# Kernel tuning notes

Measured on AMD Instinct MI355X. Metric: run time of the kernel, lower is better.

Reference implementation:

```python
import jax, jax.numpy as jnp
import numpy as np

B, S, E, H = 4, 2048, 1024, 16
D = E // H  # head dim


def setup_inputs() -> dict:
    key = jax.random.key(0)
    ks = jax.random.split(key, 6)
    sc = 1.0 / np.sqrt(E)
    return {
        "x":  jax.random.normal(ks[0], (B, S, E), dtype=jnp.float32),
        "Wk": jax.random.normal(ks[1], (E, E), dtype=jnp.float32) * sc,
        "Wq": jax.random.normal(ks[2], (E, E), dtype=jnp.float32) * sc,
        "Wv": jax.random.normal(ks[3], (E, E), dtype=jnp.float32) * sc,
        "Wo": jax.random.normal(ks[4], (E, E), dtype=jnp.float32) * sc,
        "bo": jax.random.normal(ks[5], (E,), dtype=jnp.float32) * sc,
    }


def reference(x, Wk, Wq, Wv, Wo, bo):
    b, s, e = x.shape
    # torch Linear: y = x @ W.T (weights are [out, in])
    K = x @ Wk.T
    Q = x @ Wq.T
    _V_unused = x @ Wv.T  # computed in source but discarded (V = Q.view bug)
    # split heads: [b, s, H, D] -> [b, H, s, D]
    Kh = K.reshape(b, s, H, D).transpose(0, 2, 1, 3)
    Qh = Q.reshape(b, s, H, D).transpose(0, 2, 1, 3)
    Vh = Qh  # faithful to source: V = Q.view(...)
    # scaled dot product, scaled by sqrt(embedding_size) as in source
    scores = jnp.einsum('bhqd,bhkd->bhqk', Qh, Kh) / jnp.sqrt(jnp.float32(e))
    causal = jnp.tril(jnp.ones((s, s), dtype=bool))
    scores = jnp.where(causal, scores, -jnp.inf)
    probs = jax.nn.softmax(scores, axis=-1)
    attn = jnp.einsum('bhqk,bhkd->bhqd', probs, Vh)
    attn = attn.transpose(0, 2, 1, 3).reshape(b, s, e)
    return attn @ Wo.T + bo
```

## Files before the change

kernel.cpp:

```cpp
#include <hip/hip_runtime.h>
#include <hip/hip_bf16.h>

#define PB 4
#define PS 2048
#define PE 1024
#define PH 16
#define PD 64

typedef __attribute__((ext_vector_type(8))) short bf16x8;
typedef __attribute__((ext_vector_type(4))) float f32x4;
typedef const __attribute__((address_space(1))) unsigned int* gas_t;
typedef __attribute__((address_space(3))) unsigned int* las_t;

__device__ __forceinline__ unsigned short f2bf(float f) {
  union { float f; unsigned int u; } v;
  v.f = f;
  unsigned int u = v.u;
  u += 0x7fffu + ((u >> 16) & 1u);
  return (unsigned short)(u >> 16);
}

__device__ __forceinline__ f32x4 mfma16(bf16x8 a, bf16x8 b, f32x4 c) {
  return __builtin_amdgcn_mfma_f32_16x16x32_bf16(a, b, c, 0, 0, 0);
}

#define CVT_GROUPS ((PB * PS * PE + 3 * PE * PE) / 4)
#define CVT_BLOCKS (CVT_GROUPS / 256)
__global__ __launch_bounds__(256) void cvt_kernel(
    const float* __restrict__ x, const float* __restrict__ wk,
    const float* __restrict__ wq, const float* __restrict__ wo,
    unsigned short* __restrict__ xb, unsigned short* __restrict__ wkb,
    unsigned short* __restrict__ wqb, unsigned short* __restrict__ wob) {
  const long long NX = (long long)PB * PS * PE;
  const long long NW = (long long)PE * PE;
  long long i = ((long long)blockIdx.x * 256 + threadIdx.x) * 4;
  const float* src;
  unsigned short* dst;
  long long off;
  if (i < NX)               { src = x;  dst = xb;  off = i; }
  else if (i < NX + NW)     { src = wk; dst = wkb; off = i - NX; }
  else if (i < NX + 2 * NW) { src = wq; dst = wqb; off = i - NX - NW; }
  else                      { src = wo; dst = wob; off = i - NX - 2 * NW; }
  float4 v = *(const float4*)(src + off);
  ushort4 o;
  o.x = f2bf(v.x); o.y = f2bf(v.y); o.z = f2bf(v.z); o.w = f2bf(v.w);
  *(ushort4*)(dst + off) = o;
}

__global__ __launch_bounds__(256) void gemm_qk(
    const unsigned short* __restrict__ A, const unsigned short* __restrict__ Bq,
    const unsigned short* __restrict__ Bk,
    unsigned short* __restrict__ QT, unsigned short* __restrict__ Kb) {
  const int K = PE, N = PE;
  __shared__ __attribute__((aligned(16))) unsigned short As[128 * 64];
  __shared__ __attribute__((aligned(16))) unsigned short Bqs[128 * 64];
  __shared__ __attribute__((aligned(16))) unsigned short Bks[128 * 64];
  const int tid = threadIdx.x;
  const int wave = tid >> 6, lane = tid & 63;
  const int quad = lane >> 4, ln = lane & 15;
  const int m0 = blockIdx.y * 128, n0 = blockIdx.x * 128;
  const int wm = (wave >> 1) * 64, wn = (wave & 1) * 64;

  f32x4 aq[4][4], ak[4][4];
#pragma unroll
  for (int i = 0; i < 4; ++i)
#pragma unroll
    for (int j = 0; j < 4; ++j)
#pragma unroll
      for (int r = 0; r < 4; ++r) { aq[i][j][r] = 0.f; ak[i][j][r] = 0.f; }

  for (int k0 = 0; k0 < K; k0 += 64) {
#pragma unroll
    for (int it = 0; it < 4; ++it) {
      const int idx = it * 256 + tid;
      const int row = idx >> 3, ch = idx & 7;
      const int gch = ch ^ (row & 7);
      __builtin_amdgcn_global_load_lds(
          (gas_t)(const void*)(A + (size_t)(m0 + row) * K + k0 + gch * 8),
          (las_t)(void*)((char*)As + idx * 16), 16, 0, 0);
      __builtin_amdgcn_global_load_lds(
          (gas_t)(const void*)(Bq + (size_t)(n0 + row) * K + k0 + gch * 8),
          (las_t)(void*)((char*)Bqs + idx * 16), 16, 0, 0);
      __builtin_amdgcn_global_load_lds(
          (gas_t)(const void*)(Bk + (size_t)(n0 + row) * K + k0 + gch * 8),
          (las_t)(void*)((char*)Bks + idx * 16), 16, 0, 0);
    }
    __syncthreads();
#pragma unroll
    for (int kc = 0; kc < 2; ++kc) {
      bf16x8 af[4], bqf[4], bkf[4];
#pragma unroll
      for (int t = 0; t < 4; ++t) {
        const int ra = wm + t * 16 + ln;
        const int rb = wn + t * 16 + ln;
        af[t]  = *(const bf16x8*)(As  + ra * 64 + ((kc * 4 + quad) ^ (ra & 7)) * 8);
        bqf[t] = *(const bf16x8*)(Bqs + rb * 64 + ((kc * 4 + quad) ^ (rb & 7)) * 8);
        bkf[t] = *(const bf16x8*)(Bks + rb * 64 + ((kc * 4 + quad) ^ (rb & 7)) * 8);
      }
#pragma unroll
      for (int mt = 0; mt < 4; ++mt)
#pragma unroll
        for (int nt = 0; nt < 4; ++nt) {
          aq[mt][nt] = mfma16(af[mt], bqf[nt], aq[mt][nt]);
          ak[mt][nt] = mfma16(af[mt], bkf[nt], ak[mt][nt]);
        }
    }
    __syncthreads();
  }

#pragma unroll
  for (int mt = 0; mt < 4; ++mt) {
#pragma unroll
    for (int nt = 0; nt < 4; ++nt) {
      const int row = m0 + wm + mt * 16 + quad * 4;
      const int col = n0 + wn + nt * 16 + ln;
      const int b = row >> 11, s = row & 2047;
      const int h = col >> 6, d = col & 63;
      ushort4 ov;
      ov.x = f2bf(aq[mt][nt][0]); ov.y = f2bf(aq[mt][nt][1]);
      ov.z = f2bf(aq[mt][nt][2]); ov.w = f2bf(aq[mt][nt][3]);
      *(ushort4*)(QT + (((size_t)(b * PH + h) * PD + d) * PS + s)) = ov;
#pragma unroll
      for (int r = 0; r < 4; ++r)
        Kb[(size_t)(row + r) * N + col] = f2bf(ak[mt][nt][r]);
    }
  }
}

__global__ __launch_bounds__(256) void gemm_out(
    const unsigned short* __restrict__ A, const unsigned short* __restrict__ Bm,
    const float* __restrict__ bias, float* __restrict__ Cf) {
  const int K = PE, N = PE;
  __shared__ __attribute__((aligned(16))) unsigned short As[128 * 64];
  __shared__ __attribute__((aligned(16))) unsigned short Bs[128 * 64];
  const int tid = threadIdx.x;
  const int wave = tid >> 6, lane = tid & 63;
  const int quad = lane >> 4, ln = lane & 15;
  const int m0 = blockIdx.y * 128, n0 = blockIdx.x * 128;
  const int wm = (wave >> 1) * 64, wn = (wave & 1) * 64;

  f32x4 acc[4][4];
#pragma unroll
  for (int i = 0; i < 4; ++i)
#pragma unroll
    for (int j = 0; j < 4; ++j)
#pragma unroll
      for (int r = 0; r < 4; ++r) acc[i][j][r] = 0.f;

  for (int k0 = 0; k0 < K; k0 += 64) {
#pragma unroll
    for (int it = 0; it < 4; ++it) {
      const int idx = it * 256 + tid;
      const int row = idx >> 3, ch = idx & 7;
      const int gch = ch ^ (row & 7);
      __builtin_amdgcn_global_load_lds(
          (gas_t)(const void*)(A + (size_t)(m0 + row) * K + k0 + gch * 8),
          (las_t)(void*)((char*)As + idx * 16), 16, 0, 0);
      __builtin_amdgcn_global_load_lds(
          (gas_t)(const void*)(Bm + (size_t)(n0 + row) * K + k0 + gch * 8),
          (las_t)(void*)((char*)Bs + idx * 16), 16, 0, 0);
    }
    __syncthreads();
#pragma unroll
    for (int kc = 0; kc < 2; ++kc) {
      bf16x8 af[4], bfr[4];
#pragma unroll
      for (int t = 0; t < 4; ++t) {
        const int ra = wm + t * 16 + ln;
        const int rb = wn + t * 16 + ln;
        af[t]  = *(const bf16x8*)(As + ra * 64 + ((kc * 4 + quad) ^ (ra & 7)) * 8);
        bfr[t] = *(const bf16x8*)(Bs + rb * 64 + ((kc * 4 + quad) ^ (rb & 7)) * 8);
      }
#pragma unroll
      for (int mt = 0; mt < 4; ++mt)
#pragma unroll
        for (int nt = 0; nt < 4; ++nt)
          acc[mt][nt] = mfma16(af[mt], bfr[nt], acc[mt][nt]);
    }
    __syncthreads();
  }

#pragma unroll
  for (int mt = 0; mt < 4; ++mt) {
#pragma unroll
    for (int nt = 0; nt < 4; ++nt) {
      const int row = m0 + wm + mt * 16 + quad * 4;
      const int col = n0 + wn + nt * 16 + ln;
      const float bv = bias[col];
#pragma unroll
      for (int r = 0; r < 4; ++r)
        Cf[(size_t)(row + r) * N + col] = acc[mt][nt][r] + bv;
    }
  }
}

__global__ __launch_bounds__(256) void attn_kernel(
    const unsigned short* __restrict__ QT,
    const unsigned short* __restrict__ Kb,
    unsigned short* __restrict__ Ab) {
  __shared__ __attribute__((aligned(16))) unsigned short Ks[64 * 64];
  __shared__ __attribute__((aligned(16))) unsigned short Vs[64 * 64];
  __shared__ __attribute__((aligned(16))) unsigned short Ps[4][32 * 72];

  const int tid = threadIdx.x;
  const int wave = tid >> 6, lane = tid & 63;
  const int quad = lane >> 4, ln = lane & 15;
  const int h = blockIdx.y, b = blockIdx.z;
  const size_t hoff  = ((size_t)b * PS) * PE + (size_t)h * PD;
  const size_t hofft = ((size_t)(b * PH + h) * PD) * PS;
  const float CEXP = 0.045084220f;
  const int srow = tid >> 3, sch = tid & 7;

  for (int pass = 0; pass < 2; ++pass) {
    const int qt = pass ? (int)blockIdx.x : 15 - (int)blockIdx.x;
    const int qw0 = qt * 128 + wave * 32;

    bf16x8 qfr[2][2];
#pragma unroll
    for (int nq = 0; nq < 2; ++nq)
#pragma unroll
      for (int c = 0; c < 2; ++c) {
        union { unsigned short u[8]; bf16x8 v; } tmp;
#pragma unroll
        for (int j = 0; j < 8; ++j)
          tmp.u[j] = QT[hofft + (size_t)(c * 32 + quad * 8 + j) * PS +
                        qw0 + nq * 16 + ln];
        qfr[nq][c] = tmp.v;
      }

    f32x4 o[2][4];
    float psum[2];
#pragma unroll
    for (int mq = 0; mq < 2; ++mq)
#pragma unroll
      for (int td = 0; td < 4; ++td)
#pragma unroll
        for (int r = 0; r < 4; ++r) o[mq][td][r] = 0.f;
    psum[0] = psum[1] = 0.f;

    const int ktend = 2 * qt + 2;
    for (int kt = 0; kt < ktend; ++kt) {
      const int k0 = kt * 64;

#pragma unroll
      for (int r = 0; r < 2; ++r) {
        const int row = r * 32 + srow;
        const int gch = sch ^ (row & 7);
        __builtin_amdgcn_global_load_lds(
            (gas_t)(const void*)(Kb + hoff + (size_t)(k0 + row) * PE + gch * 8),
            (las_t)(void*)((char*)Ks + (r * 256 + tid) * 16), 16, 0, 0);
        __builtin_amdgcn_global_load_lds(
            (gas_t)(const void*)(QT + hofft + (size_t)row * PS + k0 + gch * 8),
            (las_t)(void*)((char*)Vs + (r * 256 + tid) * 16), 16, 0, 0);
      }
      __syncthreads();

      f32x4 sacc[4][2];
#pragma unroll
      for (int mk = 0; mk < 4; ++mk)
#pragma unroll
        for (int nq = 0; nq < 2; ++nq)
#pragma unroll
          for (int r = 0; r < 4; ++r) sacc[mk][nq][r] = 0.f;
#pragma unroll
      for (int c = 0; c < 2; ++c) {
        const int ch = ((c * 4 + quad) ^ (ln & 7)) * 8;
        bf16x8 kf[4];
#pragma unroll
        for (int mk = 0; mk < 4; ++mk)
          kf[mk] = *(const bf16x8*)(Ks + (mk * 16 + ln) * 64 + ch);
#pragma unroll
        for (int mk = 0; mk < 4; ++mk)
#pragma unroll
          for (int nq = 0; nq < 2; ++nq)
            sacc[mk][nq] = mfma16(kf[mk], qfr[nq][c], sacc[mk][nq]);
      }

      const bool edge = (k0 + 63) > qw0;
#pragma unroll
      for (int mk = 0; mk < 4; ++mk)
#pragma unroll
        for (int nq = 0; nq < 2; ++nq) {
          float p[4];
#pragma unroll
          for (int r = 0; r < 4; ++r)
            p[r] = __builtin_amdgcn_exp2f(sacc[mk][nq][r] * CEXP);
          if (edge) {
            const int qg = qw0 + nq * 16 + ln;
#pragma unroll
            for (int r = 0; r < 4; ++r) {
              const int kg = k0 + mk * 16 + quad * 4 + r;
              p[r] = (kg <= qg) ? p[r] : 0.f;
            }
          }
          psum[nq] += (p[0] + p[1]) + (p[2] + p[3]);
          union { __hip_bfloat162 h2; unsigned int u; } u01, u23;
          u01.h2 = __float22bfloat162_rn(float2{p[0], p[1]});
          u23.h2 = __float22bfloat162_rn(float2{p[2], p[3]});
          *(uint2*)(&Ps[wave][(nq * 16 + ln) * 72 + mk * 16 + quad * 4]) =
              uint2{u01.u, u23.u};
        }

#pragma unroll
      for (int c = 0; c < 2; ++c) {
        const int ch = ((c * 4 + quad) ^ (ln & 7)) * 8;
        bf16x8 pf0 = *(const bf16x8*)(&Ps[wave][ln * 72 + c * 32 + quad * 8]);
        bf16x8 pf1 = *(const bf16x8*)(&Ps[wave][(16 + ln) * 72 + c * 32 + quad * 8]);
#pragma unroll
        for (int td = 0; td < 4; ++td) {
          bf16x8 vfd = *(const bf16x8*)(Vs + (td * 16 + ln) * 64 + ch);
          o[0][td] = mfma16(pf0, vfd, o[0][td]);
          o[1][td] = mfma16(pf1, vfd, o[1][td]);
        }
      }
      __syncthreads();
    }

#pragma unroll
    for (int nq = 0; nq < 2; ++nq) {
      psum[nq] += __shfl_xor(psum[nq], 16, 64);
      psum[nq] += __shfl_xor(psum[nq], 32, 64);
    }
    float invq[2][4];
#pragma unroll
    for (int mq = 0; mq < 2; ++mq)
#pragma unroll
      for (int r = 0; r < 4; ++r)
        invq[mq][r] = 1.f / __shfl(psum[mq], quad * 4 + r, 64);

#pragma unroll
    for (int mq = 0; mq < 2; ++mq)
#pragma unroll
      for (int r = 0; r < 4; ++r) {
        const int qg = qw0 + mq * 16 + quad * 4 + r;
#pragma unroll
        for (int td = 0; td < 4; ++td)
          Ab[hoff + (size_t)qg * PE + td * 16 + ln] =
              f2bf(o[mq][td][r] * invq[mq][r]);
      }
  }
}

extern "C" void kernel_launch(void* const* d_in, const int* in_sizes, int n_in,
                              void* d_out, int out_size, void* d_ws, size_t ws_size,
                              hipStream_t stream) {
  (void)in_sizes; (void)n_in; (void)out_size; (void)ws_size;
  const float* x  = (const float*)d_in[0];
  const float* Wk = (const float*)d_in[1];
  const float* Wq = (const float*)d_in[2];
  const float* Wo = (const float*)d_in[4];
  const float* bo = (const float*)d_in[5];
  float* out = (float*)d_out;

  char* ws = (char*)d_ws;
  unsigned short* xb  = (unsigned short*)(ws);
  unsigned short* wkb = (unsigned short*)(ws + (16u << 20));
  unsigned short* wqb = (unsigned short*)(ws + (18u << 20));
  unsigned short* wob = (unsigned short*)(ws + (20u << 20));
  unsigned short* QT  = (unsigned short*)(ws + (22u << 20));
  unsigned short* Kb  = (unsigned short*)(ws + (38u << 20));
  unsigned short* Ab  = xb;

  const int M = PB * PS;

  cvt_kernel<<<dim3(CVT_BLOCKS), dim3(256), 0, stream>>>(
      x, Wk, Wq, Wo, xb, wkb, wqb, wob);

  gemm_qk<<<dim3(PE / 128, M / 128), dim3(256), 0, stream>>>(
      xb, wqb, wkb, QT, Kb);

  attn_kernel<<<dim3(8, PH, PB), dim3(256), 0, stream>>>(QT, Kb, Ab);

  gemm_out<<<dim3(PE / 128, M / 128), dim3(256), 0, stream>>>(
      Ab, wob, bo, out);
}
```

Baseline: 262.0 us.

## Double-buffer LDS tiles in GEMM and attention kernels to overlap loads

Adds ping-pong shared-memory buffers to the QK projection GEMM, the output GEMM, and the attention loop, so the next tile's global-to-LDS load is issued before the current tile is computed. One barrier per iteration replaces the two it had before. The GEMMs halve their K-step to 32 with a new 4-chunk swizzle, which keeps LDS size the same but doubles the iteration count. Attention LDS grows, which may reduce occupancy.

```diff
diff --git a/kernel.cpp b/kernel.cpp
--- a/kernel.cpp
+++ b/kernel.cpp
@@ -52,9 +52,9 @@
     const unsigned short* __restrict__ Bk,
     unsigned short* __restrict__ QT, unsigned short* __restrict__ Kb) {
   const int K = PE, N = PE;
-  __shared__ __attribute__((aligned(16))) unsigned short As[128 * 64];
-  __shared__ __attribute__((aligned(16))) unsigned short Bqs[128 * 64];
-  __shared__ __attribute__((aligned(16))) unsigned short Bks[128 * 64];
+  __shared__ __attribute__((aligned(16))) unsigned short As[2][128 * 32];
+  __shared__ __attribute__((aligned(16))) unsigned short Bqs[2][128 * 32];
+  __shared__ __attribute__((aligned(16))) unsigned short Bks[2][128 * 32];
   const int tid = threadIdx.x;
   const int wave = tid >> 6, lane = tid & 63;
   const int quad = lane >> 4, ln = lane & 15;
@@ -69,43 +69,49 @@
 #pragma unroll
       for (int r = 0; r < 4; ++r) { aq[i][j][r] = 0.f; ak[i][j][r] = 0.f; }
 
-  for (int k0 = 0; k0 < K; k0 += 64) {
-#pragma unroll
-    for (int it = 0; it < 4; ++it) {
+  auto stage = [&](int k0, int bufi) {
+#pragma unroll
+    for (int it = 0; it < 2; ++it) {
       const int idx = it * 256 + tid;
-      const int row = idx >> 3, ch = idx & 7;
-      const int gch = ch ^ (row & 7);
+      const int row = it * 64 + (tid >> 2), ch = tid & 3;
+      const int gch = ch ^ ((row >> 1) & 3);
       __builtin_amdgcn_global_load_lds(
           (gas_t)(const void*)(A + (size_t)(m0 + row) * K + k0 + gch * 8),
-          (las_t)(void*)((char*)As + idx * 16), 16, 0, 0);
+          (las_t)(void*)((char*)As[bufi] + idx * 16), 16, 0, 0);
       __builtin_amdgcn_global_load_lds(
           (gas_t)(const void*)(Bq + (size_t)(n0 + row) * K + k0 + gch * 8),
-          (las_t)(void*)((char*)Bqs + idx * 16), 16, 0, 0);
+          (las_t)(void*)((char*)Bqs[bufi] + idx * 16), 16, 0, 0);
       __builtin_amdgcn_global_load_lds(
           (gas_t)(const void*)(Bk + (size_t)(n0 + row) * K + k0 + gch * 8),
-          (las_t)(void*)((char*)Bks + idx * 16), 16, 0, 0);
-    }
+          (las_t)(void*)((char*)Bks[bufi] + idx * 16), 16, 0, 0);
+    }
+  };
+
+  stage(0, 0);
+  for (int k0 = 0, kit = 0; k0 < K; k0 += 32, ++kit) {
     __syncthreads();
-#pragma unroll
-    for (int kc = 0; kc < 2; ++kc) {
-      bf16x8 af[4], bqf[4], bkf[4];
-#pragma unroll
-      for (int t = 0; t < 4; ++t) {
-        const int ra = wm + t * 16 + ln;
-        const int rb = wn + t * 16 + ln;
-        af[t]  = *(const bf16x8*)(As  + ra * 64 + ((kc * 4 + quad) ^ (ra & 7)) * 8);
-        bqf[t] = *(const bf16x8*)(Bqs + rb * 64 + ((kc * 4 + quad) ^ (rb & 7)) * 8);
-        bkf[t] = *(const bf16x8*)(Bks + rb * 64 + ((kc * 4 + quad) ^ (rb & 7)) * 8);
-      }
-#pragma unroll
-      for (int mt = 0; mt < 4; ++mt)
-#pragma unroll
-        for (int nt = 0; nt < 4; ++nt) {
-          aq[mt][nt] = mfma16(af[mt], bqf[nt], aq[mt][nt]);
-          ak[mt][nt] = mfma16(af[mt], bkf[nt], ak[mt][nt]);
-        }
-    }
-    __syncthreads();
+    if (k0 + 32 < K) stage(k0 + 32, (kit + 1) & 1);
+    const unsigned short* as  = As[kit & 1];
+    const unsigned short* bqs = Bqs[kit & 1];
+    const unsigned short* bks = Bks[kit & 1];
+    bf16x8 af[4], bqf[4], bkf[4];
+#pragma unroll
+    for (int t = 0; t < 4; ++t) {
+      const int ra = wm + t * 16 + ln;
+      const int rb = wn + t * 16 + ln;
+      const int sa = quad ^ ((ra >> 1) & 3);
+      const int sb = quad ^ ((rb >> 1) & 3);
+      af[t]  = *(const bf16x8*)(as  + ra * 32 + sa * 8);
+      bqf[t] = *(const bf16x8*)(bqs + rb * 32 + sb * 8);
+      bkf[t] = *(const bf16x8*)(bks + rb * 32 + sb * 8);
+    }
+#pragma unroll
+    for (int mt = 0; mt < 4; ++mt)
+#pragma unroll
+      for (int nt = 0; nt < 4; ++nt) {
+        aq[mt][nt] = mfma16(af[mt], bqf[nt], aq[mt][nt]);
+        ak[mt][nt] = mfma16(af[mt], bkf[nt], ak[mt][nt]);
+      }
   }
 
 #pragma unroll
@@ -131,8 +137,8 @@
     const unsigned short* __restrict__ A, const unsigned short* __restrict__ Bm,
     const float* __restrict__ bias, float* __restrict__ Cf) {
   const int K = PE, N = PE;
-  __shared__ __attribute__((aligned(16))) unsigned short As[128 * 64];
-  __shared__ __attribute__((aligned(16))) unsigned short Bs[128 * 64];
+  __shared__ __attribute__((aligned(16))) unsigned short As[2][128 * 32];
+  __shared__ __attribute__((aligned(16))) unsigned short Bs[2][128 * 32];
   const int tid = threadIdx.x;
   const int wave = tid >> 6, lane = tid & 63;
   const int quad = lane >> 4, ln = lane & 15;
@@ -147,37 +153,40 @@
 #pragma unroll
       for (int r = 0; r < 4; ++r) acc[i][j][r] = 0.f;
 
-  for (int k0 = 0; k0 < K; k0 += 64) {
-#pragma unroll
-    for (int it = 0; it < 4; ++it) {
+  auto stage = [&](int k0, int bufi) {
+#pragma unroll
+    for (int it = 0; it < 2; ++it) {
       const int idx = it * 256 + tid;
-      const int row = idx >> 3, ch = idx & 7;
-      const int gch = ch ^ (row & 7);
+      const int row = it * 64 + (tid >> 2), ch = tid & 3;
+      const int gch = ch ^ ((row >> 1) & 3);
       __builtin_amdgcn_global_load_lds(
           (gas_t)(const void*)(A + (size_t)(m0 + row) * K + k0 + gch * 8),
-          (las_t)(void*)((char*)As + idx * 16), 16, 0, 0);
+          (las_t)(void*)((char*)As[bufi] + idx * 16), 16, 0, 0);
       __builtin_amdgcn_global_load_lds(
           (gas_t)(const void*)(Bm + (size_t)(n0 + row) * K + k0 + gch * 8),
-          (las_t)(void*)((char*)Bs + idx * 16), 16, 0, 0);
-    }
+          (las_t)(void*)((char*)Bs[bufi] + idx * 16), 16, 0, 0);
+    }
+  };
+
+  stage(0, 0);
+  for (int k0 = 0, kit = 0; k0 < K; k0 += 32, ++kit) {
     __syncthreads();
-#pragma unroll
-    for (int kc = 0; kc < 2; ++kc) {
-      bf16x8 af[4], bfr[4];
-#pragma unroll
-      for (int t = 0; t < 4; ++t) {
-        const int ra = wm + t * 16 + ln;
-        const int rb = wn + t * 16 + ln;
-        af[t]  = *(const bf16x8*)(As + ra * 64 + ((kc * 4 + quad) ^ (ra & 7)) * 8);
-        bfr[t] = *(const bf16x8*)(Bs + rb * 64 + ((kc * 4 + quad) ^ (rb & 7)) * 8);
-      }
-#pragma unroll
-      for (int mt = 0; mt < 4; ++mt)
-#pragma unroll
-        for (int nt = 0; nt < 4; ++nt)
-          acc[mt][nt] = mfma16(af[mt], bfr[nt], acc[mt][nt]);
-    }
-    __syncthreads();
+    if (k0 + 32 < K) stage(k0 + 32, (kit + 1) & 1);
+    const unsigned short* as = As[kit & 1];
+    const unsigned short* bs = Bs[kit & 1];
+    bf16x8 af[4], bfr[4];
+#pragma unroll
+    for (int t = 0; t < 4; ++t) {
+      const int ra = wm + t * 16 + ln;
+      const int rb = wn + t * 16 + ln;
+      af[t]  = *(const bf16x8*)(as + ra * 32 + (quad ^ ((ra >> 1) & 3)) * 8);
+      bfr[t] = *(const bf16x8*)(bs + rb * 32 + (quad ^ ((rb >> 1) & 3)) * 8);
+    }
+#pragma unroll
+    for (int mt = 0; mt < 4; ++mt)
+#pragma unroll
+      for (int nt = 0; nt < 4; ++nt)
+        acc[mt][nt] = mfma16(af[mt], bfr[nt], acc[mt][nt]);
   }
 
 #pragma unroll
@@ -198,8 +207,8 @@
     const unsigned short* __restrict__ QT,
     const unsigned short* __restrict__ Kb,
     unsigned short* __restrict__ Ab) {
-  __shared__ __attribute__((aligned(16))) unsigned short Ks[64 * 64];
-  __shared__ __attribute__((aligned(16))) unsigned short Vs[64 * 64];
+  __shared__ __attribute__((aligned(16))) unsigned short Ks[2][64 * 64];
+  __shared__ __attribute__((aligned(16))) unsigned short Vs[2][64 * 64];
   __shared__ __attribute__((aligned(16))) unsigned short Ps[4][32 * 72];
 
   const int tid = threadIdx.x;
@@ -211,6 +220,20 @@
   const float CEXP = 0.045084220f;
   const int srow = tid >> 3, sch = tid & 7;
 
+  auto stage = [&](int k0, int bufi) {
+#pragma unroll
+    for (int r = 0; r < 2; ++r) {
+      const int row = r * 32 + srow;
+      const int gch = sch ^ (row & 7);
+      __builtin_amdgcn_global_load_lds(
+          (gas_t)(const void*)(Kb + hoff + (size_t)(k0 + row) * PE + gch * 8),
+          (las_t)(void*)((char*)Ks[bufi] + (r * 256 + tid) * 16), 16, 0, 0);
+      __builtin_amdgcn_global_load_lds(
+          (gas_t)(const void*)(QT + hofft + (size_t)row * PS + k0 + gch * 8),
+          (las_t)(void*)((char*)Vs[bufi] + (r * 256 + tid) * 16), 16, 0, 0);
+    }
+  };
+
   for (int pass = 0; pass < 2; ++pass) {
     const int qt = pass ? (int)blockIdx.x : 15 - (int)blockIdx.x;
     const int qw0 = qt * 128 + wave * 32;
@@ -239,21 +262,13 @@
     psum[0] = psum[1] = 0.f;
 
     const int ktend = 2 * qt + 2;
+    stage(0, 0);
     for (int kt = 0; kt < ktend; ++kt) {
+      __syncthreads();
+      if (kt + 1 < ktend) stage((kt + 1) * 64, (kt + 1) & 1);
       const int k0 = kt * 64;
-
-#pragma unroll
-      for (int r = 0; r < 2; ++r) {
-        const int row = r * 32 + srow;
-        const int gch = sch ^ (row & 7);
-        __builtin_amdgcn_global_load_lds(
-            (gas_t)(const void*)(Kb + hoff + (size_t)(k0 + row) * PE + gch * 8),
-            (las_t)(void*)((char*)Ks + (r * 256 + tid) * 16), 16, 0, 0);
-        __builtin_amdgcn_global_load_lds(
-            (gas_t)(const void*)(QT + hofft + (size_t)row * PS + k0 + gch * 8),
-            (las_t)(void*)((char*)Vs + (r * 256 + tid) * 16), 16, 0, 0);
-      }
-      __syncthreads();
+      const unsigned short* ks = Ks[kt & 1];
+      const unsigned short* vs = Vs[kt & 1];
 
       f32x4 sacc[4][2];
 #pragma unroll
@@ -268,7 +283,7 @@
         bf16x8 kf[4];
 #pragma unroll
         for (int mk = 0; mk < 4; ++mk)
-          kf[mk] = *(const bf16x8*)(Ks + (mk * 16 + ln) * 64 + ch);
+          kf[mk] = *(const bf16x8*)(ks + (mk * 16 + ln) * 64 + ch);
 #pragma unroll
         for (int mk = 0; mk < 4; ++mk)
 #pragma unroll
@@ -308,12 +323,11 @@
         bf16x8 pf1 = *(const bf16x8*)(&Ps[wave][(16 + ln) * 72 + c * 32 + quad * 8]);
 #pragma unroll
         for (int td = 0; td < 4; ++td) {
-          bf16x8 vfd = *(const bf16x8*)(Vs + (td * 16 + ln) * 64 + ch);
+          bf16x8 vfd = *(const bf16x8*)(vs + (td * 16 + ln) * 64 + ch);
           o[0][td] = mfma16(pf0, vfd, o[0][td]);
           o[1][td] = mfma16(pf1, vfd, o[1][td]);
         }
       }
-      __syncthreads();
     }
 
 #pragma unroll
```

Result: slower. 272.4 us (+4.0%).
